# Kernel optimization log

Hardware: AMD Instinct MI355X
Metric: run time of the kernel (lower is better)

Reference implementation:

```python
import jax, jax.numpy as jnp
import numpy as np

NEG_INF = -1e30
EPS = 1e-6


def _apply_rope_interleaved(x, cos, sin):
    # x: (..., rope_dim); cos/sin broadcastable to (..., rope_dim//2)
    x1 = x[..., 0::2]
    x2 = x[..., 1::2]
    o1 = x1 * cos - x2 * sin
    o2 = x1 * sin + x2 * cos
    return jnp.stack([o1, o2], axis=-1).reshape(x.shape)


def setup_inputs() -> dict:
    key = jax.random.key(0)
    ks = jax.random.split(key, 6)
    B, S, D = 1, 2048, 7168
    H, HD, ROPE, QLR = 64, 128, 64, 1536
    x = jax.random.normal(ks[0], (B, S, D), dtype=jnp.float32)
    q_lora = jax.random.normal(ks[1], (B, S, QLR), dtype=jnp.float32)
    wq_b = jax.random.normal(ks[2], (QLR, H * HD), dtype=jnp.float32) * 0.02
    wk = jax.random.normal(ks[3], (D, HD), dtype=jnp.float32) * 0.02
    weights_proj = jax.random.normal(ks[4], (D, H), dtype=jnp.float32) * 0.02
    k_norm_w = jnp.ones((HD,), dtype=jnp.float32)
    k_norm_b = jnp.zeros((HD,), dtype=jnp.float32)
    # standard RoPE tables for the first ROPE dims
    half = ROPE // 2
    inv_freq = 1.0 / (10000.0 ** (np.arange(half, dtype=np.float64) / half))
    ang = np.arange(S, dtype=np.float64)[:, None] * inv_freq[None, :]
    cos = jnp.asarray(np.cos(ang), dtype=jnp.float32)
    sin = jnp.asarray(np.sin(ang), dtype=jnp.float32)
    return {"x": x, "q_lora": q_lora, "wq_b": wq_b, "wk": wk,
            "weights_proj": weights_proj, "k_norm_w": k_norm_w,
            "k_norm_b": k_norm_b, "cos": cos, "sin": sin, "topk": 512}


def reference(x, q_lora, wq_b, wk, weights_proj, k_norm_w, k_norm_b, cos, sin, topk):
    B, S, D = x.shape
    HD = wk.shape[1]
    H = weights_proj.shape[1]
    ROPE = cos.shape[1] * 2
    # queries: low-rank up-projection -> per-head, RoPE on first ROPE dims
    q = (q_lora @ wq_b).reshape(B, S, H, HD)
    q_pe = _apply_rope_interleaved(q[..., :ROPE], cos[None, :, None, :], sin[None, :, None, :])
    q = jnp.concatenate([q_pe, q[..., ROPE:]], axis=-1)
    # keys: single head, LayerNorm then RoPE on first ROPE dims
    k = x @ wk  # [B,S,HD]
    mu = k.mean(-1, keepdims=True)
    var = ((k - mu) ** 2).mean(-1, keepdims=True)
    k = (k - mu) * jax.lax.rsqrt(var + EPS) * k_norm_w + k_norm_b
    k_pe = _apply_rope_interleaved(k[..., :ROPE], cos[None], sin[None])
    k = jnp.concatenate([k_pe, k[..., ROPE:]], axis=-1)
    # per-token head gates, scaled by n_heads^-0.5 and softmax scale HD^-0.5
    w = (x @ weights_proj) * (H ** -0.5) * (HD ** -0.5)  # [B,S,H]
    # lightning index score: I[t,s] = sum_h w[t,h] * relu(q[t,h] . k[s])
    scores = jax.nn.relu(jnp.einsum('bshd,btd->bsht', q, k))  # [B,S,H,S]
    index_score = jnp.einsum('bsht,bsh->bst', scores, w)      # [B,S,S]
    # causal mask then top-k token selection
    causal = jnp.arange(S)[None, :] <= jnp.arange(S)[:, None]
    index_score = jnp.where(causal[None], index_score, NEG_INF)
    vals, idx = jax.lax.top_k(index_score, topk)
    return vals, idx
```

## Files before the change

kernel.cpp:

```cpp
#include <hip/hip_runtime.h>
#include <stdint.h>

#define S_LEN 2048
#define D_DIM 7168
#define H_NUM 64
#define HD_DIM 128
#define QLR_DIM 1536
#define NQ_DIM 8192
#define ROPE_DIM 64
#define HALF_DIM 32
#define TOPK_N 512
#define NEG_INF_F (-1e30f)
#define LN_EPS 1e-6f
#define W_SCALE 0.011048543456039806f

#define KCHUNKS 7
#define KCHUNK_SZ 1024
#define NKT 24

#define QF_HSTRIDE (128 * 4 * 64 * 8)

#define QBF_OFF 0
#define ALORA_OFF (QBF_OFF + S_LEN * NQ_DIM / 2)
#define WT_OFF   (ALORA_OFF + S_LEN * QLR_DIM / 2)
#define XBF_OFF  (WT_OFF + NQ_DIM * QLR_DIM / 2)
#define WT2_OFF  (XBF_OFF + S_LEN * D_DIM / 2)
#define KF_OFF   (WT2_OFF + 192 * D_DIM / 2)
#define KBF_OFF  (KF_OFF + S_LEN * HD_DIM)
#define WF_OFF   (KBF_OFF + S_LEN * HD_DIM / 2)
#define SC_OFF   (WF_OFF + S_LEN * H_NUM)

typedef __attribute__((ext_vector_type(8))) short short8;
typedef __attribute__((ext_vector_type(4))) float floatx4;

__device__ __forceinline__ ushort f2bf(float f) {
    unsigned int u = __float_as_uint(f);
    u += 0x7FFFu + ((u >> 16) & 1u);
    return (ushort)(u >> 16);
}
__device__ __forceinline__ unsigned int pack2bf(float lo, float hi) {
    return (unsigned int)f2bf(lo) | ((unsigned int)f2bf(hi) << 16);
}

__device__ __forceinline__ void gld_lds16(const ushort* g, ushort* l) {
    __builtin_amdgcn_global_load_lds(
        (const __attribute__((address_space(1))) unsigned int*)g,
        (__attribute__((address_space(3))) unsigned int*)l, 16, 0, 0);
}

__global__ __launch_bounds__(256) void cast_bf16_kernel(
    const float* __restrict__ in, ushort* __restrict__ out)
{
    int g = (blockIdx.x * 256 + threadIdx.x) * 8;
    float4 a = *(const float4*)&in[g];
    float4 b = *(const float4*)&in[g + 4];
    uint4 v;
    v.x = pack2bf(a.x, a.y); v.y = pack2bf(a.z, a.w);
    v.z = pack2bf(b.x, b.y); v.w = pack2bf(b.z, b.w);
    *(uint4*)&out[g] = v;
}

__global__ __launch_bounds__(256) void transpose_wqb_kernel(
    const float* __restrict__ W, ushort* __restrict__ WT)
{
    __shared__ ushort tl[64][72];
    const int n0 = blockIdx.x * 64, k0 = blockIdx.y * 64;
    const int t = threadIdx.x;
    const int r = t >> 4, c4 = (t & 15) * 4;
#pragma unroll
    for (int u = 0; u < 4; u++) {
        int kk = r + u * 16;
        float4 v = *(const float4*)&W[(size_t)(k0 + kk) * NQ_DIM + n0 + c4];
        tl[c4 + 0][kk] = f2bf(v.x);
        tl[c4 + 1][kk] = f2bf(v.y);
        tl[c4 + 2][kk] = f2bf(v.z);
        tl[c4 + 3][kk] = f2bf(v.w);
    }
    __syncthreads();
#pragma unroll
    for (int u = 0; u < 2; u++) {
        int i = t + u * 256;
        int nr = i >> 3, c8 = (i & 7) * 8;
        uint4 v = *(const uint4*)&tl[nr][c8];
        *(uint4*)&WT[(size_t)(n0 + nr) * QLR_DIM + k0 + c8] = v;
    }
}

__global__ __launch_bounds__(256) void transpose_wkp_kernel(
    const float* __restrict__ WK, const float* __restrict__ WP,
    ushort* __restrict__ WT2)
{
    __shared__ ushort tl[64][72];
    const int ntile = blockIdx.x;
    const int k0 = blockIdx.y * 64;
    const float* src; int ld, cbase;
    if (ntile < 2) { src = WK; ld = HD_DIM; cbase = ntile * 64; }
    else           { src = WP; ld = H_NUM; cbase = 0; }
    const int t = threadIdx.x;
    const int r = t >> 4, c4 = (t & 15) * 4;
#pragma unroll
    for (int u = 0; u < 4; u++) {
        int kk = r + u * 16;
        float4 v = *(const float4*)&src[(size_t)(k0 + kk) * ld + cbase + c4];
        tl[c4 + 0][kk] = f2bf(v.x);
        tl[c4 + 1][kk] = f2bf(v.y);
        tl[c4 + 2][kk] = f2bf(v.z);
        tl[c4 + 3][kk] = f2bf(v.w);
    }
    __syncthreads();
#pragma unroll
    for (int u = 0; u < 2; u++) {
        int i = t + u * 256;
        int nr = i >> 3, c8 = (i & 7) * 8;
        uint4 v = *(const uint4*)&tl[nr][c8];
        *(uint4*)&WT2[(size_t)(ntile * 64 + nr) * D_DIM + k0 + c8] = v;
    }
}

__global__ __launch_bounds__(512, 2) void qgemm_mfma_kernel(
    const ushort* __restrict__ Abf,
    const ushort* __restrict__ WT,
    const float* __restrict__ cosp, const float* __restrict__ sinp,
    ushort* __restrict__ Qo)
{
    __shared__ __align__(16) ushort lds[65536];

    const int tid = threadIdx.x;
    const int lane = tid & 63;
    const int wave = tid >> 6;
    const int m = lane & 15;
    const int q = lane >> 4;
    const int wm = wave & 1;
    const int wn = wave >> 1;

    const int wg = blockIdx.x;
    const int xcd = wg & 7, lid = wg >> 3;
    const int bx = xcd * 4 + (lid & 3);
    const int by = lid >> 2;
    const int m0 = by * 256;
    const int n0 = bx * 256;

    const ushort* sgA[2][2];
    const ushort* sgB[2][2];
    unsigned int ldoff[2][2];
#pragma unroll
    for (int h = 0; h < 2; h++)
#pragma unroll
        for (int r = 0; r < 2; r++) {
            int s = r * 512 + wave * 64 + lane;
            int row = s >> 3, c = s & 7;
            int kg = c ^ (row & 7);
            sgA[h][r] = Abf + (size_t)(m0 + h * 128 + row) * QLR_DIM + kg * 8;
            sgB[h][r] = WT  + (size_t)(n0 + h * 128 + row) * QLR_DIM + kg * 8;
            ldoff[h][r] = (unsigned int)(h * 8192 + (r * 512 + wave * 64) * 8);
        }

    auto stageA = [&](int kt, int h) {
        ushort* dbase = &lds[(kt & 1) * 16384];
        gld_lds16(sgA[h][0] + kt * 64, dbase + ldoff[h][0]);
        gld_lds16(sgA[h][1] + kt * 64, dbase + ldoff[h][1]);
    };
    auto stageB = [&](int kt, int h) {
        ushort* dbase = &lds[32768 + (kt & 1) * 16384];
        gld_lds16(sgB[h][0] + kt * 64, dbase + ldoff[h][0]);
        gld_lds16(sgB[h][1] + kt * 64, dbase + ldoff[h][1]);
    };

    unsigned int aoff[2], boff[2];
#pragma unroll
    for (int ks = 0; ks < 2; ks++) {
        unsigned int xr = (unsigned int)(((((ks << 2) + q) ^ (m & 7))) * 8);
        aoff[ks] = (unsigned int)((wm * 128 + m) * 64) + xr;
        boff[ks] = (unsigned int)((wn * 64 + m) * 64) + xr;
    }

    floatx4 acc[8][4];
#pragma unroll
    for (int i = 0; i < 8; i++)
#pragma unroll
        for (int j = 0; j < 4; j++) acc[i][j] = (floatx4){0.f, 0.f, 0.f, 0.f};

    stageA(0, 0); stageA(0, 1); stageB(0, 0); stageB(0, 1);
    stageA(1, 0); stageA(1, 1);
    asm volatile("s_waitcnt vmcnt(4)" ::: "memory");
    __builtin_amdgcn_s_barrier();

    short8 af[4][2], bfr[2][2];

    for (int kt = 0; kt < NKT; ++kt) {
        const ushort* as = &lds[(kt & 1) * 16384];
        const ushort* bs = &lds[32768 + (kt & 1) * 16384];

#pragma unroll
        for (int mt = 0; mt < 4; mt++)
#pragma unroll
            for (int ks = 0; ks < 2; ks++)
                af[mt][ks] = *(const short8*)&as[aoff[ks] + mt * 1024];
#pragma unroll
        for (int nt = 0; nt < 2; nt++)
#pragma unroll
            for (int ks = 0; ks < 2; ks++)
                bfr[nt][ks] = *(const short8*)&bs[boff[ks] + nt * 1024];
        if (kt + 1 < NKT) stageB(kt + 1, 0);
        __builtin_amdgcn_s_barrier();
        asm volatile("s_waitcnt lgkmcnt(0)" ::: "memory");
        __builtin_amdgcn_s_setprio(1);
#pragma unroll
        for (int mt = 0; mt < 4; mt++)
#pragma unroll
            for (int nt = 0; nt < 2; nt++)
#pragma unroll
                for (int ks = 0; ks < 2; ks++)
                    acc[mt][nt] = __builtin_amdgcn_mfma_f32_16x16x32_bf16(
                        af[mt][ks], bfr[nt][ks], acc[mt][nt], 0, 0, 0);
        __builtin_amdgcn_s_setprio(0);
        __builtin_amdgcn_s_barrier();

#pragma unroll
        for (int nt = 0; nt < 2; nt++)
#pragma unroll
            for (int ks = 0; ks < 2; ks++)
                bfr[nt][ks] = *(const short8*)&bs[boff[ks] + 2048 + nt * 1024];
        if (kt + 1 < NKT) stageB(kt + 1, 1);
        __builtin_amdgcn_s_barrier();
        asm volatile("s_waitcnt lgkmcnt(0)" ::: "memory");
        __builtin_amdgcn_s_setprio(1);
#pragma unroll
        for (int mt = 0; mt < 4; mt++)
#pragma unroll
            for (int nt = 0; nt < 2; nt++)
#pragma unroll
                for (int ks = 0; ks < 2; ks++)
                    acc[mt][2 + nt] = __builtin_amdgcn_mfma_f32_16x16x32_bf16(
                        af[mt][ks], bfr[nt][ks], acc[mt][2 + nt], 0, 0, 0);
        __builtin_amdgcn_s_setprio(0);
        __builtin_amdgcn_s_barrier();

#pragma unroll
        for (int mt = 0; mt < 4; mt++)
#pragma unroll
            for (int ks = 0; ks < 2; ks++)
                af[mt][ks] = *(const short8*)&as[aoff[ks] + 4096 + mt * 1024];
        __builtin_amdgcn_s_barrier();
        asm volatile("s_waitcnt lgkmcnt(0)" ::: "memory");
        __builtin_amdgcn_s_setprio(1);
#pragma unroll
        for (int mt = 0; mt < 4; mt++)
#pragma unroll
            for (int nt = 0; nt < 2; nt++)
#pragma unroll
                for (int ks = 0; ks < 2; ks++)
                    acc[4 + mt][2 + nt] = __builtin_amdgcn_mfma_f32_16x16x32_bf16(
                        af[mt][ks], bfr[nt][ks], acc[4 + mt][2 + nt], 0, 0, 0);
        __builtin_amdgcn_s_setprio(0);
        __builtin_amdgcn_s_barrier();

#pragma unroll
        for (int nt = 0; nt < 2; nt++)
#pragma unroll
            for (int ks = 0; ks < 2; ks++)
                bfr[nt][ks] = *(const short8*)&bs[boff[ks] + nt * 1024];
        if (kt + 2 < NKT) { stageA(kt + 2, 0); stageA(kt + 2, 1); }
        __builtin_amdgcn_s_barrier();
        asm volatile("s_waitcnt lgkmcnt(0)" ::: "memory");
        __builtin_amdgcn_s_setprio(1);
#pragma unroll
        for (int mt = 0; mt < 4; mt++)
#pragma unroll
            for (int nt = 0; nt < 2; nt++)
#pragma unroll
                for (int ks = 0; ks < 2; ks++)
                    acc[4 + mt][nt] = __builtin_amdgcn_mfma_f32_16x16x32_bf16(
                        af[mt][ks], bfr[nt][ks], acc[4 + mt][nt], 0, 0, 0);
        __builtin_amdgcn_s_setprio(0);
        if (kt >= NKT - 2) asm volatile("s_waitcnt vmcnt(0)" ::: "memory");
        else               asm volatile("s_waitcnt vmcnt(4)" ::: "memory");
        __builtin_amdgcn_s_barrier();
    }

    __syncthreads();
    ushort* ep = lds;
    const int h0 = bx * 2;
    const int sgrp0 = m0 >> 4;

#pragma unroll
    for (int hh = 0; hh < 2; hh++) {
        if ((wn >> 1) == hh) {
            const int dbase = (wn & 1) * 64;
            const bool do_rope = ((wn & 1) == 0);
#pragma unroll
            for (int ai = 0; ai < 8; ai++) {
                const int srow0 = m0 + wm * 128 + ai * 16 + q * 4;
#pragma unroll
                for (int bj = 0; bj < 4; bj++) {
                    const int d = dbase + bj * 16 + m;
                    float o[4];
                    if (do_rope) {
                        const int jj = d >> 1;
#pragma unroll
                        for (int r = 0; r < 4; r++) {
                            float x = acc[ai][bj][r];
                            float p = __shfl_xor(x, 1, 64);
                            float c = cosp[(srow0 + r) * HALF_DIM + jj];
                            float sn = sinp[(srow0 + r) * HALF_DIM + jj];
                            o[r] = (d & 1) ? (p * sn + x * c) : (x * c - p * sn);
                        }
                    } else {
#pragma unroll
                        for (int r = 0; r < 4; r++) o[r] = acc[ai][bj][r];
                    }
#pragma unroll
                    for (int r = 0; r < 4; r++)
                        ep[(wm * 128 + ai * 16 + q * 4 + r) * 136 + d] = f2bf(o[r]);
                }
            }
        }
        __syncthreads();
        const size_t hstr = (size_t)(h0 + hh) * QF_HSTRIDE;
#pragma unroll
        for (int u = 0; u < 8; u++) {
            int i = u * 512 + tid;
            int sgl = i >> 8, c = i & 255;
            int ks = c >> 6, ln = c & 63;
            int srow = sgl * 16 + (ln & 15);
            int d0 = (ks << 5) + ((ln >> 4) << 3);
            uint4 v = *(const uint4*)&ep[srow * 136 + d0];
            *(uint4*)&Qo[hstr + ((((size_t)(sgrp0 + sgl) * 4 + ks) * 64 + ln) * 8)] = v;
        }
        __syncthreads();
    }
}

__global__ __launch_bounds__(256) void kw_mfma_kernel(
    const ushort* __restrict__ Xbf,
    const ushort* __restrict__ WT2,
    float* __restrict__ partial)
{
    __shared__ ushort As[128 * 64];
    __shared__ ushort Bs[64 * 64];

    const int tid = threadIdx.x;
    const int lane = tid & 63;
    const int wave = tid >> 6;
    const int m = lane & 15;
    const int q = lane >> 4;
    const int wm = wave & 1, wn = wave >> 1;
    const int m0 = blockIdx.x * 128;
    const int n0 = blockIdx.y * 64;
    const int kc = blockIdx.z;
    const size_t kbase = (size_t)kc * KCHUNK_SZ;

    const ushort* agp[4];
    unsigned int abase[4];
#pragma unroll
    for (int u = 0; u < 4; u++) {
        int s = (u * 4 + wave) * 64 + lane;
        int row = s >> 3, c = s & 7;
        int kg = c ^ (row & 7);
        agp[u] = Xbf + (size_t)(m0 + row) * D_DIM + kbase + kg * 8;
        abase[u] = (unsigned int)((u * 4 + wave) * 64 * 8);
    }
    const ushort* bgp[2];
    unsigned int bbase[2];
#pragma unroll
    for (int u = 0; u < 2; u++) {
        int s = (u * 4 + wave) * 64 + lane;
        int row = s >> 3, c = s & 7;
        int kg = c ^ (row & 7);
        bgp[u] = WT2 + (size_t)(n0 + row) * D_DIM + kbase + kg * 8;
        bbase[u] = (unsigned int)((u * 4 + wave) * 64 * 8);
    }

    floatx4 acc[4][2];
#pragma unroll
    for (int i = 0; i < 4; i++)
#pragma unroll
        for (int j = 0; j < 2; j++) acc[i][j] = (floatx4){0.f, 0.f, 0.f, 0.f};

    for (int kt = 0; kt < KCHUNK_SZ; kt += 64) {
        __syncthreads();
#pragma unroll
        for (int u = 0; u < 4; u++) gld_lds16(agp[u] + kt, &As[abase[u]]);
#pragma unroll
        for (int u = 0; u < 2; u++) gld_lds16(bgp[u] + kt, &Bs[bbase[u]]);
        __syncthreads();

        short8 af[4][2], bfr[2][2];
#pragma unroll
        for (int mt = 0; mt < 4; mt++) {
            int row = wm * 64 + mt * 16 + m;
#pragma unroll
            for (int ks = 0; ks < 2; ks++)
                af[mt][ks] = *(const short8*)
                    &As[row * 64 + ((((ks << 2) + q) ^ (m & 7)) * 8)];
        }
#pragma unroll
        for (int nt = 0; nt < 2; nt++) {
            int row = wn * 32 + nt * 16 + m;
#pragma unroll
            for (int ks = 0; ks < 2; ks++)
                bfr[nt][ks] = *(const short8*)
                    &Bs[row * 64 + ((((ks << 2) + q) ^ (m & 7)) * 8)];
        }
#pragma unroll
        for (int mt = 0; mt < 4; mt++)
#pragma unroll
            for (int nt = 0; nt < 2; nt++)
#pragma unroll
                for (int ks = 0; ks < 2; ks++)
                    acc[mt][nt] = __builtin_amdgcn_mfma_f32_16x16x32_bf16(
                        af[mt][ks], bfr[nt][ks], acc[mt][nt], 0, 0, 0);
    }

#pragma unroll
    for (int mt = 0; mt < 4; mt++) {
        int grow = m0 + wm * 64 + mt * 16 + q * 4;
#pragma unroll
        for (int nt = 0; nt < 2; nt++) {
            int gn = n0 + wn * 32 + nt * 16 + m;
#pragma unroll
            for (int r = 0; r < 4; r++)
                partial[((size_t)kc * S_LEN + grow + r) * 192 + gn] = acc[mt][nt][r];
        }
    }
}

__global__ __launch_bounds__(256) void kw_reduce_kernel(
    const float* __restrict__ partial, float* __restrict__ Ko, float* __restrict__ Wo)
{
    int g = blockIdx.x * 256 + threadIdx.x;
    int m = g / 192, n = g % 192;
    float s = 0.f;
#pragma unroll
    for (int c = 0; c < KCHUNKS; c++)
        s += partial[((size_t)c * S_LEN + m) * 192 + n];
    if (n < HD_DIM) Ko[(size_t)m * HD_DIM + n] = s;
    else            Wo[(size_t)m * H_NUM + (n - HD_DIM)] = s * W_SCALE;
}

__global__ __launch_bounds__(128) void knorm_rope_kernel(
    const float* __restrict__ Kf, const float* __restrict__ gw, const float* __restrict__ gb,
    const float* __restrict__ cosp, const float* __restrict__ sinp,
    ushort* __restrict__ Kbf)
{
    __shared__ float red[128];
    __shared__ float sh[128];
    const int m = blockIdx.x, t = threadIdx.x;
    float v = Kf[(size_t)m * HD_DIM + t];
    red[t] = v; __syncthreads();
    for (int off = 64; off > 0; off >>= 1) {
        if (t < off) red[t] += red[t + off];
        __syncthreads();
    }
    float mu = red[0] * (1.f / HD_DIM);
    __syncthreads();
    float dv = v - mu;
    red[t] = dv * dv; __syncthreads();
    for (int off = 64; off > 0; off >>= 1) {
        if (t < off) red[t] += red[t + off];
        __syncthreads();
    }
    float var = red[0] * (1.f / HD_DIM);
    float rs = rsqrtf(var + LN_EPS);
    float kn = dv * rs * gw[t] + gb[t];
    sh[t] = kn; __syncthreads();
    float out;
    if (t < ROPE_DIM) {
        int jj = t >> 1;
        float c = cosp[m * HALF_DIM + jj], sn = sinp[m * HALF_DIM + jj];
        out = ((t & 1) == 0) ? (sh[t] * c - sh[t + 1] * sn)
                             : (sh[t - 1] * sn + sh[t] * c);
    } else {
        out = kn;
    }
    Kbf[(size_t)m * HD_DIM + t] = f2bf(out);
}

__global__ __launch_bounds__(256, 2) void attn_mfma_kernel(
    const ushort* __restrict__ Qb,
    const ushort* __restrict__ Kb,
    const float* __restrict__ Wf,
    float* __restrict__ SC)
{
    __shared__ float Wsm[64 * 68];

    const int bidx = blockIdx.x;
    const int x = bidx & 7, j = bidx >> 3;
    const int g1 = x + 1, g2 = 32 - x, g3 = x + 9;
    int ts, tt;
    if (j < g1)                { ts = x;      tt = j; }
    else if (j < g1 + g2)      { ts = 31 - x; tt = j - g1; }
    else if (j < g1 + g2 + g3) { ts = x + 8;  tt = j - g1 - g2; }
    else                       { ts = 23 - x; tt = j - g1 - g2 - g3; }
    const int s0 = ts * 64, t0 = tt * 64;

    const int tid = threadIdx.x;
    const int lane = tid & 63;
    const int m = lane & 15;
    const int q = lane >> 4;
    const int strip = (tid >> 6) * 16;

    {
        const float4* gw = (const float4*)(Wf + (size_t)s0 * H_NUM);
#pragma unroll
        for (int u = 0; u < 4; u++) {
            int ch = tid + u * 256;
            float4 v = gw[ch];
            *(float4*)&Wsm[(ch >> 4) * 68 + (ch & 15) * 4] = v;
        }
    }

    short8 bf[4][4];
#pragma unroll
    for (int tile = 0; tile < 4; tile++)
#pragma unroll
        for (int ks = 0; ks < 4; ks++)
            bf[tile][ks] = *(const short8*)
                &Kb[(size_t)(t0 + tile * 16 + m) * HD_DIM + ks * 32 + q * 8];

    __syncthreads();

    float acc[4][4];
#pragma unroll
    for (int tile = 0; tile < 4; tile++)
#pragma unroll
        for (int r = 0; r < 4; r++) acc[tile][r] = 0.f;

    const int sgrp = ts * 4 + (strip >> 4);
    const ushort* qfb = Qb + ((size_t)sgrp * 4 * 64 + lane) * 8;
    const float* wrow = &Wsm[(strip + q * 4) * 68];

    auto loadQ = [&](short8* dst, int h) {
        const ushort* p = qfb + (size_t)h * QF_HSTRIDE;
#pragma unroll
        for (int ks = 0; ks < 4; ks++) dst[ks] = *(const short8*)&p[ks * 512];
    };
    auto computeH = [&](const short8* af, int h) {
        float wv[4];
#pragma unroll
        for (int r = 0; r < 4; r++) wv[r] = wrow[r * 68 + h];
#pragma unroll
        for (int tile = 0; tile < 4; tile++) {
            floatx4 p = {0.f, 0.f, 0.f, 0.f};
#pragma unroll
            for (int ks = 0; ks < 4; ks++)
                p = __builtin_amdgcn_mfma_f32_16x16x32_bf16(af[ks], bf[tile][ks], p, 0, 0, 0);
#pragma unroll
            for (int r = 0; r < 4; r++)
                acc[tile][r] += fmaxf(p[r], 0.f) * wv[r];
        }
    };

    short8 afA[4], afB[4];
    loadQ(afA, 0);
    for (int h = 0; h < H_NUM; h += 2) {
        loadQ(afB, h + 1);
        computeH(afA, h);
        if (h + 2 < H_NUM) loadQ(afA, h + 2);
        computeH(afB, h + 1);
    }

#pragma unroll
    for (int tile = 0; tile < 4; tile++)
#pragma unroll
        for (int r = 0; r < 4; r++)
            SC[(size_t)(s0 + strip + q * 4 + r) * S_LEN + t0 + tile * 16 + m] =
                acc[tile][r];
}

__device__ __forceinline__ unsigned int fkey(float f) {
    unsigned int u = __float_as_uint(f);
    return (u & 0x80000000u) ? ~u : (u | 0x80000000u);
}

__global__ __launch_bounds__(256) void topk_kernel(
    const float* __restrict__ SC, float* __restrict__ outv, float* __restrict__ outi)
{
    __shared__ unsigned int key[S_LEN];
    __shared__ float val[S_LEN];
    const int s = blockIdx.x, tid = threadIdx.x;
    const int nchunks = (s >> 9) + 1;
    const int nact = nchunks << 9;

    for (int t = tid; t < nact; t += 256) {
        float v = (t <= s) ? SC[(size_t)s * S_LEN + t] : NEG_INF_F;
        val[t] = v;
        key[t] = (fkey(v) & 0xFFFFF800u) | (unsigned int)(S_LEN - 1 - t);
    }
    __syncthreads();

    for (int k2 = 2; k2 <= 512; k2 <<= 1) {
        for (int j = k2 >> 1; j > 0; j >>= 1) {
            for (int p = tid; p < (nact >> 1); p += 256) {
                int i = 2 * p - (p & (j - 1));
                int il = i & 511;
                unsigned int a = key[i], b = key[i + j];
                bool up = ((il & k2) == 0);
                bool sw = up ? (a < b) : (a > b);
                if (sw) { key[i] = b; key[i + j] = a; }
            }
            __syncthreads();
        }
    }

    for (int c = 1; c < nchunks; c++) {
        for (int p = tid; p < 512; p += 256) {
            unsigned int a = key[p], b = key[(c << 9) + 511 - p];
            key[p] = a > b ? a : b;
        }
        __syncthreads();
        for (int j = 256; j > 0; j >>= 1) {
            int p = tid;
            int i = 2 * p - (p & (j - 1));
            unsigned int a = key[i], b = key[i + j];
            if (a < b) { key[i] = b; key[i + j] = a; }
            __syncthreads();
        }
    }

    for (int i2 = tid; i2 < TOPK_N; i2 += 256) {
        unsigned int kv = key[i2];
        int t = S_LEN - 1 - (int)(kv & 0x7FFu);
        outv[(size_t)s * TOPK_N + i2] = val[t];
        outi[(size_t)s * TOPK_N + i2] = (float)t;
    }
}

extern "C" void kernel_launch(void* const* d_in, const int* in_sizes, int n_in,
                              void* d_out, int out_size, void* d_ws, size_t ws_size,
                              hipStream_t stream)
{
    (void)in_sizes; (void)n_in; (void)out_size; (void)ws_size;
    const float* x      = (const float*)d_in[0];
    const float* q_lora = (const float*)d_in[1];
    const float* wq_b   = (const float*)d_in[2];
    const float* wk     = (const float*)d_in[3];
    const float* wproj  = (const float*)d_in[4];
    const float* knw    = (const float*)d_in[5];
    const float* knb    = (const float*)d_in[6];
    const float* cosp   = (const float*)d_in[7];
    const float* sinp   = (const float*)d_in[8];

    float* ws = (float*)d_ws;
    ushort* Qbf  = (ushort*)(ws + QBF_OFF);
    ushort* Albf = (ushort*)(ws + ALORA_OFF);
    ushort* WTbf = (ushort*)(ws + WT_OFF);
    ushort* Xbf  = (ushort*)(ws + XBF_OFF);
    ushort* WT2  = (ushort*)(ws + WT2_OFF);
    float*  Kf   = ws + KF_OFF;
    ushort* Kbf  = (ushort*)(ws + KBF_OFF);
    float*  Wf   = ws + WF_OFF;
    float*  SCb  = ws + SC_OFF;
    float*  partial = ws + SC_OFF;

    float* outv = (float*)d_out;
    float* outi = outv + (size_t)S_LEN * TOPK_N;

    cast_bf16_kernel<<<(S_LEN * QLR_DIM) / (256 * 8), 256, 0, stream>>>(q_lora, Albf);
    cast_bf16_kernel<<<(S_LEN * D_DIM) / (256 * 8), 256, 0, stream>>>(x, Xbf);
    transpose_wqb_kernel<<<dim3(NQ_DIM / 64, QLR_DIM / 64), 256, 0, stream>>>(wq_b, WTbf);
    transpose_wkp_kernel<<<dim3(3, D_DIM / 64), 256, 0, stream>>>(wk, wproj, WT2);
    kw_mfma_kernel<<<dim3(S_LEN / 128, 3, KCHUNKS), 256, 0, stream>>>(Xbf, WT2, partial);
    kw_reduce_kernel<<<(S_LEN * 192) / 256, 256, 0, stream>>>(partial, Kf, Wf);
    knorm_rope_kernel<<<S_LEN, 128, 0, stream>>>(Kf, knw, knb, cosp, sinp, Kbf);
    qgemm_mfma_kernel<<<256, 512, 0, stream>>>(Albf, WTbf, cosp, sinp, Qbf);
    attn_mfma_kernel<<<528, 256, 0, stream>>>(Qbf, Kbf, Wf, SCb);
    topk_kernel<<<S_LEN, 256, 0, stream>>>(SCb, outv, outi);
}
```

Measured before the change: 340.7 us.

## Restructure GEMM main loop into k-split phases with one-ahead prefetch

Reorganizes the bf16 MFMA main loop so each phase walks one k-slice across all four N tiles, rather than splitting work by N half with both k-slices held in registers. Prefetch drops from two tiles ahead for A to one tile ahead for both A and B, and each iteration ends with a full vmcnt(0) wait. The explicit lgkmcnt waits are removed and the loop is unrolled by 2. The intent is fewer live fragment registers and a simpler schedule, but shallower prefetch exposes more global-load latency. Dropping the LDS waits leans on the compiler to insert them before the MFMAs.

```diff
diff --git a/kernel.cpp b/kernel.cpp
--- a/kernel.cpp
+++ b/kernel.cpp
@@ -181,100 +181,80 @@
         for (int j = 0; j < 4; j++) acc[i][j] = (floatx4){0.f, 0.f, 0.f, 0.f};
 
     stageA(0, 0); stageA(0, 1); stageB(0, 0); stageB(0, 1);
-    stageA(1, 0); stageA(1, 1);
-    asm volatile("s_waitcnt vmcnt(4)" ::: "memory");
+    asm volatile("s_waitcnt vmcnt(0)" ::: "memory");
     __builtin_amdgcn_s_barrier();
 
-    short8 af[4][2], bfr[2][2];
-
+#pragma unroll 2
     for (int kt = 0; kt < NKT; ++kt) {
         const ushort* as = &lds[(kt & 1) * 16384];
         const ushort* bs = &lds[32768 + (kt & 1) * 16384];
-
-#pragma unroll
-        for (int mt = 0; mt < 4; mt++)
-#pragma unroll
-            for (int ks = 0; ks < 2; ks++)
-                af[mt][ks] = *(const short8*)&as[aoff[ks] + mt * 1024];
-#pragma unroll
-        for (int nt = 0; nt < 2; nt++)
-#pragma unroll
-            for (int ks = 0; ks < 2; ks++)
-                bfr[nt][ks] = *(const short8*)&bs[boff[ks] + nt * 1024];
-        if (kt + 1 < NKT) stageB(kt + 1, 0);
-        __builtin_amdgcn_s_barrier();
-        asm volatile("s_waitcnt lgkmcnt(0)" ::: "memory");
+        const bool pf = (kt + 1 < NKT);
+
+        short8 af[4], bf0[4], bf1[4];
+
+#pragma unroll
+        for (int mt = 0; mt < 4; mt++)
+            af[mt] = *(const short8*)&as[aoff[0] + mt * 1024];
+#pragma unroll
+        for (int nt = 0; nt < 4; nt++)
+            bf0[nt] = *(const short8*)&bs[boff[0] + nt * 1024];
+        if (pf) { stageA(kt + 1, 0); stageA(kt + 1, 1); stageB(kt + 1, 0); }
+        __builtin_amdgcn_s_barrier();
         __builtin_amdgcn_s_setprio(1);
 #pragma unroll
         for (int mt = 0; mt < 4; mt++)
 #pragma unroll
-            for (int nt = 0; nt < 2; nt++)
-#pragma unroll
-                for (int ks = 0; ks < 2; ks++)
-                    acc[mt][nt] = __builtin_amdgcn_mfma_f32_16x16x32_bf16(
-                        af[mt][ks], bfr[nt][ks], acc[mt][nt], 0, 0, 0);
+            for (int nt = 0; nt < 4; nt++)
+                acc[mt][nt] = __builtin_amdgcn_mfma_f32_16x16x32_bf16(
+                    af[mt], bf0[nt], acc[mt][nt], 0, 0, 0);
         __builtin_amdgcn_s_setprio(0);
         __builtin_amdgcn_s_barrier();
 
 #pragma unroll
-        for (int nt = 0; nt < 2; nt++)
-#pragma unroll
-            for (int ks = 0; ks < 2; ks++)
-                bfr[nt][ks] = *(const short8*)&bs[boff[ks] + 2048 + nt * 1024];
-        if (kt + 1 < NKT) stageB(kt + 1, 1);
-        __builtin_amdgcn_s_barrier();
-        asm volatile("s_waitcnt lgkmcnt(0)" ::: "memory");
+        for (int mt = 0; mt < 4; mt++)
+            af[mt] = *(const short8*)&as[aoff[1] + mt * 1024];
+#pragma unroll
+        for (int nt = 0; nt < 4; nt++)
+            bf1[nt] = *(const short8*)&bs[boff[1] + nt * 1024];
+        if (pf) stageB(kt + 1, 1);
+        __builtin_amdgcn_s_barrier();
         __builtin_amdgcn_s_setprio(1);
 #pragma unroll
         for (int mt = 0; mt < 4; mt++)
 #pragma unroll
-            for (int nt = 0; nt < 2; nt++)
-#pragma unroll
-                for (int ks = 0; ks < 2; ks++)
-                    acc[mt][2 + nt] = __builtin_amdgcn_mfma_f32_16x16x32_bf16(
-                        af[mt][ks], bfr[nt][ks], acc[mt][2 + nt], 0, 0, 0);
+            for (int nt = 0; nt < 4; nt++)
+                acc[mt][nt] = __builtin_amdgcn_mfma_f32_16x16x32_bf16(
+                    af[mt], bf1[nt], acc[mt][nt], 0, 0, 0);
         __builtin_amdgcn_s_setprio(0);
         __builtin_amdgcn_s_barrier();
 
 #pragma unroll
         for (int mt = 0; mt < 4; mt++)
-#pragma unroll
-            for (int ks = 0; ks < 2; ks++)
-                af[mt][ks] = *(const short8*)&as[aoff[ks] + 4096 + mt * 1024];
-        __builtin_amdgcn_s_barrier();
-        asm volatile("s_waitcnt lgkmcnt(0)" ::: "memory");
+            af[mt] = *(const short8*)&as[aoff[0] + 4096 + mt * 1024];
+        __builtin_amdgcn_s_barrier();
         __builtin_amdgcn_s_setprio(1);
 #pragma unroll
         for (int mt = 0; mt < 4; mt++)
 #pragma unroll
-            for (int nt = 0; nt < 2; nt++)
-#pragma unroll
-                for (int ks = 0; ks < 2; ks++)
-                    acc[4 + mt][2 + nt] = __builtin_amdgcn_mfma_f32_16x16x32_bf16(
-                        af[mt][ks], bfr[nt][ks], acc[4 + mt][2 + nt], 0, 0, 0);
+            for (int nt = 0; nt < 4; nt++)
+                acc[4 + mt][nt] = __builtin_amdgcn_mfma_f32_16x16x32_bf16(
+                    af[mt], bf0[nt], acc[4 + mt][nt], 0, 0, 0);
         __builtin_amdgcn_s_setprio(0);
         __builtin_amdgcn_s_barrier();
 
 #pragma unroll
-        for (int nt = 0; nt < 2; nt++)
-#pragma unroll
-            for (int ks = 0; ks < 2; ks++)
-                bfr[nt][ks] = *(const short8*)&bs[boff[ks] + nt * 1024];
-        if (kt + 2 < NKT) { stageA(kt + 2, 0); stageA(kt + 2, 1); }
-        __builtin_amdgcn_s_barrier();
-        asm volatile("s_waitcnt lgkmcnt(0)" ::: "memory");
+        for (int mt = 0; mt < 4; mt++)
+            af[mt] = *(const short8*)&as[aoff[1] + 4096 + mt * 1024];
+        __builtin_amdgcn_s_barrier();
         __builtin_amdgcn_s_setprio(1);
 #pragma unroll
         for (int mt = 0; mt < 4; mt++)
 #pragma unroll
-            for (int nt = 0; nt < 2; nt++)
-#pragma unroll
-                for (int ks = 0; ks < 2; ks++)
-                    acc[4 + mt][nt] = __builtin_amdgcn_mfma_f32_16x16x32_bf16(
-                        af[mt][ks], bfr[nt][ks], acc[4 + mt][nt], 0, 0, 0);
+            for (int nt = 0; nt < 4; nt++)
+                acc[4 + mt][nt] = __builtin_amdgcn_mfma_f32_16x16x32_bf16(
+                    af[mt], bf1[nt], acc[4 + mt][nt], 0, 0, 0);
         __builtin_amdgcn_s_setprio(0);
-        if (kt >= NKT - 2) asm volatile("s_waitcnt vmcnt(0)" ::: "memory");
-        else               asm volatile("s_waitcnt vmcnt(4)" ::: "memory");
+        asm volatile("s_waitcnt vmcnt(0)" ::: "memory");
         __builtin_amdgcn_s_barrier();
     }
 
```

New measurement: 340.0 us. No clear change (-0.2%).
